# Optimization experiments

Measured on AMD Instinct MI355X. Metric: run time of the kernel, lower is better.

## Reference

```python
import jax, jax.numpy as jnp
import numpy as np

N, E, IN, H, OUT = 50000, 600000, 256, 128, 40
EPS, GAMMA = 0.1, 0.1  # PyG AntiSymmetricConv defaults


def _build_norm(edge_index, n):
    # GCNConv normalization with added self loops: D^-1/2 (A+I) D^-1/2
    loops = jnp.arange(n, dtype=edge_index.dtype)
    src = jnp.concatenate([edge_index[0], loops])
    dst = jnp.concatenate([edge_index[1], loops])
    deg = jax.ops.segment_sum(jnp.ones(src.shape[0], dtype=jnp.float32), dst, num_segments=n)
    dinv = jnp.where(deg > 0, jax.lax.rsqrt(jnp.maximum(deg, 1e-12)), 0.0)
    return src, dst, dinv[src] * dinv[dst]


def _gcn(x, w, src, dst, norm, n):
    # GCNConv(bias=False): scatter normalized messages to target nodes
    m = (x @ w)[src] * norm[:, None]          # [E+N, d]
    return jax.ops.segment_sum(m, dst, num_segments=n)


def _antisym_conv(x, W, gcn_w, bias, src, dst, norm, num_iters):
    d = W.shape[0]
    aW = W - W.T - GAMMA * jnp.eye(d, dtype=W.dtype)  # antisymmetric weight
    n = x.shape[0]

    def step(h, _):
        upd = jnp.tanh(h @ aW.T + _gcn(h, gcn_w, src, dst, norm, n) + bias)
        return h + EPS * upd, None

    x, _ = jax.lax.scan(step, x, None, length=num_iters)
    return x


def setup_inputs() -> dict:
    key = jax.random.key(0)
    ks = jax.random.split(key, 16)
    s = lambda fan: 1.0 / np.sqrt(fan)
    return {
        "x": jax.random.normal(ks[0], (N, IN), dtype=jnp.float32),
        "edge_index": jax.random.randint(ks[1], (2, E), 0, N, dtype=jnp.int64),
        "w_hid": jax.random.normal(ks[2], (H, IN), dtype=jnp.float32) * s(IN),
        "b_hid": jax.random.normal(ks[3], (H,), dtype=jnp.float32) * s(IN),
        "W_a1": jax.random.normal(ks[4], (H, H), dtype=jnp.float32) * s(H),
        "gcn_w1": jax.random.normal(ks[5], (H, H), dtype=jnp.float32) * s(H),
        "b_a1": jax.random.normal(ks[6], (H,), dtype=jnp.float32) * s(H),
        "w_hid2": jax.random.normal(ks[7], (H // 2, H), dtype=jnp.float32) * s(H),
        "b_hid2": jax.random.normal(ks[8], (H // 2,), dtype=jnp.float32) * s(H),
        "W_a2": jax.random.normal(ks[9], (H // 2, H // 2), dtype=jnp.float32) * s(H // 2),
        "gcn_w2": jax.random.normal(ks[10], (H // 2, H // 2), dtype=jnp.float32) * s(H // 2),
        "b_a2": jax.random.normal(ks[11], (H // 2,), dtype=jnp.float32) * s(H // 2),
        "w_fc": jax.random.normal(ks[12], (OUT, H // 2), dtype=jnp.float32) * s(H // 2),
        "b_fc": jax.random.normal(ks[13], (OUT,), dtype=jnp.float32) * s(H // 2),
    }


def reference(x, edge_index, w_hid, b_hid, W_a1, gcn_w1, b_a1,
              w_hid2, b_hid2, W_a2, gcn_w2, b_a2, w_fc, b_fc):
    n = x.shape[0]
    src, dst, norm = _build_norm(edge_index, n)
    h = jax.nn.leaky_relu(x @ w_hid.T + b_hid)          # dropout is no-op in eval
    h = _antisym_conv(h, W_a1, gcn_w1, b_a1, src, dst, norm, num_iters=3)
    h = jax.nn.leaky_relu(h)
    h = jax.nn.leaky_relu(h @ w_hid2.T + b_hid2)
    h = _antisym_conv(h, W_a2, gcn_w2, b_a2, src, dst, norm, num_iters=1)
    out = h @ w_fc.T + b_fc
    return jax.nn.log_softmax(out, axis=1)
```

## Files before the change

kernel.cpp:

```cpp
#include <hip/hip_runtime.h>
#include <hip/hip_bf16.h>
#include <math.h>

typedef unsigned short u16;
typedef unsigned int   u32;
using short8  = __attribute__((ext_vector_type(8))) short;
using f32x4   = __attribute__((ext_vector_type(4))) float;

static constexpr int NNODE = 50000;
static constexpr int NEDGE = 600000;
static constexpr float EPSC   = 0.1f;
static constexpr float GAMMAC = 0.1f;

static constexpr int NTILE = (NNODE + 63) / 64;
static constexpr int GH    = 128;
static constexpr int NRNG  = 12500;
static constexpr int NWORD = NRNG / 2;
static constexpr int NPASS = 4;

static constexpr long long O_DINV   = 0;
static constexpr long long O_DEGI   = 50000;
static constexpr long long O_ROWPTR = 100000;
static constexpr long long O_GCUR   = 150004;
static constexpr long long O_ECSR   = 200260;
static constexpr long long O_WHB    = 1400260;
static constexpr long long O_G1TB   = O_WHB  + 16384;
static constexpr long long O_AW1B   = O_G1TB + 8192;
static constexpr long long O_W2B    = O_AW1B + 8192;
static constexpr long long O_AW2B   = O_W2B  + 4096;
static constexpr long long O_G2TB   = O_AW2B + 2048;
static constexpr long long O_WFCB   = O_G2TB + 2048;
static constexpr long long O_AGGB   = 3450004;
static constexpr long long O_HB0    = O_AGGB + 3200000;
static constexpr long long O_HB1    = O_HB0  + 3200000;
static constexpr long long O_S0     = O_HB1  + 3200000;
static constexpr long long O_S1     = O_S0   + 1600000;
static constexpr long long O_PART   = O_S1   + 1600000;
static constexpr long long O_BASE   = O_PART + 3200000;

__device__ __forceinline__ float bf2f(u16 u) {
    return __uint_as_float(((unsigned)u) << 16);
}
__device__ __forceinline__ u16 f2bf(float f) {
    unsigned u = __float_as_uint(f);
    return (u16)((u + 0x7FFFu + ((u >> 16) & 1u)) >> 16);
}
__device__ __forceinline__ float ftanh(float x) {
    float x2 = fminf(fmaxf(2.f * x, -30.f), 30.f);
    float e = __expf(x2);
    return (e - 1.f) * __builtin_amdgcn_rcpf(e + 1.f);
}
__device__ __forceinline__ u16 pk_fp8(float a, float b) {
    int pk = __builtin_amdgcn_cvt_pk_fp8_f32(a, b, 0, false);
    return (u16)(pk & 0xffff);
}
__device__ __forceinline__ void acc_fp8x4(float* a, u32 v, float w) {
    a[0] += __builtin_amdgcn_cvt_f32_fp8(v, 0) * w;
    a[1] += __builtin_amdgcn_cvt_f32_fp8(v, 1) * w;
    a[2] += __builtin_amdgcn_cvt_f32_fp8(v, 2) * w;
    a[3] += __builtin_amdgcn_cvt_f32_fp8(v, 3) * w;
}

__global__ __launch_bounds__(256) void prep_kernel(
    const float* __restrict__ w_hid, const float* __restrict__ W_a1,
    const float* __restrict__ gcn1,  const float* __restrict__ w2,
    const float* __restrict__ W_a2,  const float* __restrict__ gcn2,
    const float* __restrict__ wfc,   float* __restrict__ ws)
{
    int j = blockIdx.x * 256 + threadIdx.x;
    if (j < 32768) { ((u16*)(ws+O_WHB))[j] = f2bf(w_hid[j]); return; } j -= 32768;
    if (j < 16384) { int r=j>>7, c=j&127; ((u16*)(ws+O_G1TB))[j] = f2bf(gcn1[c*128+r]); return; } j -= 16384;
    if (j < 16384) { int r=j>>7, c=j&127;
                     ((u16*)(ws+O_AW1B))[j] = f2bf(W_a1[r*128+c] - W_a1[c*128+r] - (r==c?GAMMAC:0.f));
                     return; } j -= 16384;
    if (j < 8192)  { ((u16*)(ws+O_W2B))[j] = f2bf(w2[j]); return; } j -= 8192;
    if (j < 4096)  { int r=j>>6, c=j&63;
                     ((u16*)(ws+O_AW2B))[j] = f2bf(W_a2[r*64+c] - W_a2[c*64+r] - (r==c?GAMMAC:0.f));
                     return; } j -= 4096;
    if (j < 4096)  { int r=j>>6, c=j&63; ((u16*)(ws+O_G2TB))[j] = f2bf(gcn2[c*64+r]); return; } j -= 4096;
    if (j < 2560)  { ((u16*)(ws+O_WFCB))[j] = f2bf(wfc[j]); return; } j -= 2560;
    if (j == 0)    { ((int*)(ws+O_GCUR))[0] = 0; }
}

__global__ __launch_bounds__(256) void alloc_kernel(
    const u16* __restrict__ part, float* __restrict__ dinv,
    int* __restrict__ degi, int* __restrict__ rowptr,
    u16* __restrict__ base16, int* __restrict__ gcur)
{
    int i = blockIdx.x * 256 + threadIdx.x;
    int lane = threadIdx.x & 63;
    bool ok = i < NNODE;
    int deg = 0;
    if (ok) {
        int run = 0;
        #pragma unroll 4
        for (int g = 0; g < GH; ++g) {
            base16[(long long)g * NNODE + i] = (u16)run;
            run += part[(long long)g * NNODE + i];
        }
        deg = run;
        degi[i] = deg;
        dinv[i] = rsqrtf(1.0f + (float)deg);
    }
    int run = deg;
    #pragma unroll
    for (int off = 1; off < 64; off <<= 1) {
        int v = __shfl_up(run, off);
        if (lane >= off) run += v;
    }
    int tot = __shfl(run, 63);
    int basep = 0;
    if (lane == 63) basep = atomicAdd(gcur, tot);
    basep = __shfl(basep, 63);
    if (ok) rowptr[i] = basep + run - deg;
}

__global__ __launch_bounds__(256) void fill_kernel(
    const int* __restrict__ ei, const float* __restrict__ dinv,
    const int* __restrict__ rowptr, const u16* __restrict__ base16,
    int2* __restrict__ ecsr)
{
    __shared__ u32 cur[NWORD];
    const int g    = blockIdx.x >> 2;
    const int pass = blockIdx.x & 3;
    const long long e0 = (long long)g * NEDGE / GH;
    const long long e1 = (long long)(g + 1) * NEDGE / GH;
    const u16* bb = base16 + (long long)g * NNODE;
    const int nbase = pass * NRNG;
    for (int wi = threadIdx.x; wi < NWORD; wi += 256) cur[wi] = 0;
    __syncthreads();
    for (long long e = e0 + threadIdx.x; e < e1; e += 256) {
        int d = ei[NEDGE + e];
        int r = d - nbase;
        if ((unsigned)r < (unsigned)NRNG) {
            int s = ei[e];
            u32 old = atomicAdd(&cur[r >> 1], 1u << ((r & 1) * 16));
            int rank = (int)((old >> ((r & 1) * 16)) & 0xffffu);
            int slot = rowptr[d] + (int)bb[d] + rank;
            int2 v;
            v.x = s;
            v.y = __float_as_int(dinv[s]);
            ecsr[slot] = v;
        }
    }
}

template<int KS, int NT, int AF32, int LOADACT, int EPI>
__global__ __launch_bounds__(256, 4) void mgemm(
    const void* __restrict__ Araw,
    const u16* __restrict__ Bt,
    const float* __restrict__ bias,
    float* __restrict__ outF,
    u16* __restrict__ outB,
    u16* __restrict__ outB8,
    int M, int Nn, int ldc,
    const int* __restrict__ ei,
    u16* __restrict__ partial)
{
    constexpr int K    = KS * 32;
    constexpr int KCHU = (K > 128) ? 128 : K;
    constexpr int KC   = KCHU / 32;
    constexpr int NCH  = K / KCHU;
    constexpr int P    = KCHU + 8;
    constexpr int ROWS = NT * 16;
    constexpr int CW   = NT * 16 + 1;
    constexpr int BSZ  = ROWS * P * 2;
    constexpr int ASZ  = 64 * CW * 4;
    constexpr int SMEM = BSZ > ASZ ? BSZ : ASZ;
    __shared__ __align__(16) char smem[SMEM];

    if (ei && blockIdx.x >= NTILE) {
        int g = blockIdx.x - NTILE;
        u32* hist = (u32*)smem;
        const long long e0 = (long long)g * NEDGE / GH;
        const long long e1 = (long long)(g + 1) * NEDGE / GH;
        u16* part = partial + (long long)g * NNODE;
        for (int pass = 0; pass < NPASS; ++pass) {
            const int nbase = pass * NRNG;
            for (int wi = threadIdx.x; wi < NWORD; wi += 256) hist[wi] = 0;
            __syncthreads();
            for (long long e = e0 + threadIdx.x; e < e1; e += 256) {
                int d = ei[NEDGE + e];
                int r = d - nbase;
                if ((unsigned)r < (unsigned)NRNG)
                    atomicAdd(&hist[r >> 1], 1u << ((r & 1) * 16));
            }
            __syncthreads();
            for (int wi = threadIdx.x; wi < NWORD; wi += 256)
                *(u32*)&part[nbase + wi * 2] = hist[wi];
            __syncthreads();
        }
        return;
    }

    u16*   bl   = (u16*)smem;
    float* accL = (float*)smem;

    const int wave = threadIdx.x >> 6;
    const int lane = threadIdx.x & 63;
    const int m = lane & 15, q = lane >> 4;
    const int rowbase = blockIdx.x * 64 + wave * 16;
    const int row = rowbase + m;
    const bool rok = row < M;
    const short8 z8 = {0,0,0,0,0,0,0,0};

    short8 af[KS];
    if (AF32) {
        const float* apf = (const float*)Araw + (long long)row * K;
        #pragma unroll
        for (int k = 0; k < KS; ++k) {
            short8 t = z8;
            if (rok) {
                const float4* p = (const float4*)(apf + (k * 4 + q) * 8);
                float4 a = p[0], b = p[1];
                t[0]=(short)f2bf(a.x); t[1]=(short)f2bf(a.y); t[2]=(short)f2bf(a.z); t[3]=(short)f2bf(a.w);
                t[4]=(short)f2bf(b.x); t[5]=(short)f2bf(b.y); t[6]=(short)f2bf(b.z); t[7]=(short)f2bf(b.w);
            }
            af[k] = t;
        }
    } else {
        const short8* ap = (const short8*)((const u16*)Araw + (long long)row * K);
        #pragma unroll
        for (int k = 0; k < KS; ++k) af[k] = rok ? ap[k * 4 + q] : z8;
    }
    if (LOADACT) {
        #pragma unroll
        for (int k = 0; k < KS; ++k)
            #pragma unroll
            for (int e = 0; e < 8; ++e) {
                float f = bf2f((u16)af[k][e]);
                f = f > 0.f ? f : 0.01f * f;
                af[k][e] = (short)f2bf(f);
            }
    }

    f32x4 acc[NT];
    #pragma unroll
    for (int j = 0; j < NT; ++j) acc[j] = (f32x4){0.f,0.f,0.f,0.f};

    for (int ch = 0; ch < NCH; ++ch) {
        if (ch) __syncthreads();
        constexpr int CHUNKS = ROWS * (KCHU / 8);
        for (int t = threadIdx.x; t < CHUNKS; t += 256) {
            int r = t / (KCHU / 8), c = t - r * (KCHU / 8);
            short8 v = z8;
            if (r < Nn) v = *(const short8*)&Bt[(long long)r * K + ch * KCHU + c * 8];
            *(short8*)&bl[r * P + c * 8] = v;
        }
        __syncthreads();
        #pragma unroll
        for (int j = 0; j < NT; ++j) {
            #pragma unroll
            for (int k = 0; k < KC; ++k) {
                short8 bf_ = *(const short8*)&bl[(j * 16 + m) * P + k * 32 + q * 8];
                acc[j] = __builtin_amdgcn_mfma_f32_16x16x32_bf16(af[ch * KC + k], bf_, acc[j], 0, 0, 0);
            }
        }
    }

    __syncthreads();
    #pragma unroll
    for (int j = 0; j < NT; ++j)
        #pragma unroll
        for (int r = 0; r < 4; ++r)
            accL[(wave * 16 + q * 4 + r) * CW + j * 16 + m] = acc[j][r];
    __syncthreads();

    const int c0 = lane * 2;
    if (c0 < NT * 16) {
        float2 bv = {0.f, 0.f};
        if (bias) {
            if (c0 < Nn)     bv.x = bias[c0];
            if (c0 + 1 < Nn) bv.y = bias[c0 + 1];
        }
        #pragma unroll
        for (int rl = 0; rl < 16; ++rl) {
            int rowD = rowbase + rl;
            if (rowD >= M) continue;
            float2 v = *(const float2*)&accL[(wave * 16 + rl) * CW + c0];
            long long o = (long long)rowD * ldc + c0;
            v.x += bv.x; v.y += bv.y;
            if (EPI == 1) {
                v.x = v.x > 0.f ? v.x : 0.01f * v.x;
                v.y = v.y > 0.f ? v.y : 0.01f * v.y;
            }
            if (c0 + 1 < Nn) {
                if (outB) { ushort2 ob; ob.x = f2bf(v.x); ob.y = f2bf(v.y);
                            *(ushort2*)&outB[o] = ob; }
                if (outB8) outB8[o >> 1] = pk_fp8(v.x, v.y);
                if (outF) { *(float2*)&outF[o] = v; }
            } else if (c0 < Nn) {
                if (outB) outB[o] = f2bf(v.x);
                if (outF) outF[o] = v.x;
            }
        }
    }
}

template<int HD>
__global__ __launch_bounds__(256) void gather_kernel(
    const int* __restrict__ rowptr, const int* __restrict__ degi,
    const int2* __restrict__ ecsr, const float* __restrict__ dinv,
    const u32* __restrict__ g8, u16* __restrict__ aggB)
{
    int node = (blockIdx.x * 256 + threadIdx.x) >> 6;
    int lane = threadIdx.x & 63;
    if (node >= NNODE) return;
    const int qr = lane >> 4, l4 = lane & 15;
    const int r0 = rowptr[node];
    const int r1 = r0 + degi[node];
    const float dn = dinv[node];
    constexpr int EL = (HD == 128) ? 8 : 4;

    float a[EL];
    #pragma unroll
    for (int i = 0; i < EL; ++i) a[i] = 0.f;
    if (qr == 0) {
        if (HD == 128) {
            uint2 gv = ((const uint2*)g8)[(long long)node * 16 + l4];
            acc_fp8x4(a, gv.x, dn);
            acc_fp8x4(a + 4, gv.y, dn);
        } else {
            u32 gv = g8[(long long)node * 16 + l4];
            acc_fp8x4(a, gv, dn);
        }
    }

    for (int base = r0; base < r1; base += 64) {
        int idx = base + lane;
        int cs = 0; float cw = 0.f;
        if (idx < r1) { int2 ev = ecsr[idx]; cs = ev.x; cw = __int_as_float(ev.y); }
        int cnt = min(64, r1 - base);
        for (int j = 0; j < cnt; j += 16) {
            #pragma unroll
            for (int u = 0; u < 4; ++u) {
                int jj = j + u * 4 + qr;
                int   s = __shfl(cs, jj);
                float w = __shfl(cw, jj);
                if (HD == 128) {
                    uint2 gv = ((const uint2*)g8)[(long long)s * 16 + l4];
                    acc_fp8x4(a, gv.x, w);
                    acc_fp8x4(a + 4, gv.y, w);
                } else {
                    u32 gv = g8[(long long)s * 16 + l4];
                    acc_fp8x4(a, gv, w);
                }
            }
        }
    }

    #pragma unroll
    for (int i = 0; i < EL; ++i) {
        a[i] += __shfl_xor(a[i], 16);
        a[i] += __shfl_xor(a[i], 32);
    }
    if (HD == 128) {
        float v0 = (qr == 0) ? a[0] : (qr == 1) ? a[2] : (qr == 2) ? a[4] : a[6];
        float v1 = (qr == 0) ? a[1] : (qr == 1) ? a[3] : (qr == 2) ? a[5] : a[7];
        v0 *= dn; v1 *= dn;
        long long o = (long long)node * 128 + l4 * 8 + qr * 2;
        ushort2 ob; ob.x = f2bf(v0); ob.y = f2bf(v1);
        *(ushort2*)&aggB[o] = ob;
    } else {
        float v = (qr == 0) ? a[0] : (qr == 1) ? a[1] : (qr == 2) ? a[2] : a[3];
        aggB[(long long)node * 64 + l4 * 4 + qr] = f2bf(v * dn);
    }
}

template<int TAIL>
__global__ __launch_bounds__(512, 3) void fconv(
    const u16* __restrict__ hA, const u32* __restrict__ g8,
    const int* __restrict__ rowptr, const int* __restrict__ degi,
    const int2* __restrict__ ecsr, const float* __restrict__ dinv,
    const u16* __restrict__ BtW, const u16* __restrict__ BtG,
    const float* __restrict__ bias,
    u16* __restrict__ outB, u16* __restrict__ outB8,
    const u16* __restrict__ w2W, const float* __restrict__ b2)
{
    constexpr int K = 128, P = 136;
    __shared__ __align__(16) char smem[52224];
    u16* bl   = (u16*)smem;
    u16* aggT = (u16*)(smem + 34816);
    const int wave = threadIdx.x >> 6, lane = threadIdx.x & 63;
    const int m = lane & 15, q = lane >> 4;
    const int blockrow = blockIdx.x * 64;
    const short8 z8 = {0,0,0,0,0,0,0,0};

    {
        const int qr = q, l4 = m;
        for (int nn = 0; nn < 8; ++nn) {
            int lr = wave * 8 + nn;
            int node = blockrow + lr;
            if (node >= NNODE) break;
            const int r0 = rowptr[node];
            const int r1 = r0 + degi[node];
            const float dn = dinv[node];
            float a[8] = {0.f,0.f,0.f,0.f,0.f,0.f,0.f,0.f};
            if (qr == 0) {
                uint2 gv = ((const uint2*)g8)[(long long)node * 16 + l4];
                acc_fp8x4(a, gv.x, dn);
                acc_fp8x4(a + 4, gv.y, dn);
            }
            for (int base = r0; base < r1; base += 64) {
                int idx = base + lane;
                int cs = 0; float cw = 0.f;
                if (idx < r1) { int2 ev = ecsr[idx]; cs = ev.x; cw = __int_as_float(ev.y); }
                int cnt = min(64, r1 - base);
                for (int j = 0; j < cnt; j += 16) {
                    #pragma unroll
                    for (int u = 0; u < 4; ++u) {
                        int jj = j + u * 4 + qr;
                        int   s = __shfl(cs, jj);
                        float w = __shfl(cw, jj);
                        uint2 gv = ((const uint2*)g8)[(long long)s * 16 + l4];
                        acc_fp8x4(a, gv.x, w);
                        acc_fp8x4(a + 4, gv.y, w);
                    }
                }
            }
            #pragma unroll
            for (int i = 0; i < 8; ++i) {
                a[i] += __shfl_xor(a[i], 16);
                a[i] += __shfl_xor(a[i], 32);
            }
            float v0 = (qr == 0) ? a[0] : (qr == 1) ? a[2] : (qr == 2) ? a[4] : a[6];
            float v1 = (qr == 0) ? a[1] : (qr == 1) ? a[3] : (qr == 2) ? a[5] : a[7];
            v0 *= dn; v1 *= dn;
            ushort2 ob; ob.x = f2bf(v0); ob.y = f2bf(v1);
            *(ushort2*)&aggT[lr * P + l4 * 8 + qr * 2] = ob;
        }
    }
    __syncthreads();

    const int nh = wave >> 2;
    const int rowbase = blockrow + (wave & 3) * 16;
    const int row = rowbase + m;
    const bool rok = row < NNODE;

    short8 af1[4], af2[4];
    {
        const short8* ap1 = (const short8*)(hA + (long long)row * K);
        #pragma unroll
        for (int k = 0; k < 4; ++k) {
            af1[k] = rok ? ap1[k * 4 + q] : z8;
            af2[k] = rok ? *(const short8*)&aggT[((wave & 3) * 16 + m) * P + k * 32 + q * 8] : z8;
        }
    }

    f32x4 acc[4];
    #pragma unroll
    for (int j = 0; j < 4; ++j) acc[j] = (f32x4){0.f,0.f,0.f,0.f};

    #pragma unroll
    for (int pass = 0; pass < 2; ++pass) {
        const u16* Bsrc = pass ? BtG : BtW;
        if (pass) __syncthreads();
        for (int t = threadIdx.x; t < 2048; t += 512) {
            int r = t >> 4, c = t & 15;
            *(short8*)&bl[r * P + c * 8] = *(const short8*)&Bsrc[(long long)r * K + c * 8];
        }
        __syncthreads();
        #pragma unroll
        for (int j = 0; j < 4; ++j)
            #pragma unroll
            for (int kk = 0; kk < 4; ++kk) {
                short8 b_ = *(const short8*)&bl[(nh*64 + j*16 + m) * P + kk*32 + q*8];
                acc[j] = __builtin_amdgcn_mfma_f32_16x16x32_bf16(
                    pass ? af2[kk] : af1[kk], b_, acc[j], 0, 0, 0);
            }
    }

    __syncthreads();
    float* accW = (float*)smem + wave * 16 * 65;
    #pragma unroll
    for (int j = 0; j < 4; ++j)
        #pragma unroll
        for (int r = 0; r < 4; ++r)
            accW[(q*4 + r) * 65 + j*16 + m] = acc[j][r];

    const int hw = lane >> 5;
    const int c0 = (lane & 31) * 2;
    float2 bv = {bias[nh*64 + c0], bias[nh*64 + c0 + 1]};

    if (TAIL == 0) {
        #pragma unroll
        for (int rl8 = 0; rl8 < 8; ++rl8) {
            int rl = hw * 8 + rl8;
            int rowD = rowbase + rl;
            if (rowD >= NNODE) continue;
            float2 v = *(const float2*)&accW[rl * 65 + c0];
            long long o = (long long)rowD * 128 + nh*64 + c0;
            ushort2 hh = *(const ushort2*)&hA[o];
            float n0 = bf2f(hh.x) + EPSC * ftanh(v.x + bv.x);
            float n1 = bf2f(hh.y) + EPSC * ftanh(v.y + bv.y);
            ushort2 ob; ob.x = f2bf(n0); ob.y = f2bf(n1);
            *(ushort2*)&outB[o] = ob;
            outB8[o >> 1] = pk_fp8(n0, n1);
        }
        return;
    }

    #pragma unroll
    for (int rl8 = 0; rl8 < 8; ++rl8) {
        int rl = hw * 8 + rl8;
        int rowD = rowbase + rl;
        float n0 = 0.f, n1 = 0.f;
        if (rowD < NNODE) {
            float2 v = *(const float2*)&accW[rl * 65 + c0];
            long long o = (long long)rowD * 128 + nh*64 + c0;
            ushort2 hh = *(const ushort2*)&hA[o];
            n0 = bf2f(hh.x) + EPSC * ftanh(v.x + bv.x);
            n1 = bf2f(hh.y) + EPSC * ftanh(v.y + bv.y);
            n0 = n0 > 0.f ? n0 : 0.01f * n0;
            n1 = n1 > 0.f ? n1 : 0.01f * n1;
        }
        ushort2 ob; ob.x = f2bf(n0); ob.y = f2bf(n1);
        *(ushort2*)&aggT[((wave & 3) * 16 + rl) * P + nh*64 + c0] = ob;
    }
    __syncthreads();

    short8 af3[4];
    #pragma unroll
    for (int k = 0; k < 4; ++k)
        af3[k] = *(const short8*)&aggT[((wave & 3) * 16 + m) * P + k * 32 + q * 8];

    for (int t = threadIdx.x; t < 1024; t += 512) {
        int r = t >> 4, c = t & 15;
        *(short8*)&bl[r * P + c * 8] = *(const short8*)&w2W[(long long)r * K + c * 8];
    }
    __syncthreads();

    f32x4 acc2[2];
    #pragma unroll
    for (int j = 0; j < 2; ++j) acc2[j] = (f32x4){0.f,0.f,0.f,0.f};
    #pragma unroll
    for (int j = 0; j < 2; ++j)
        #pragma unroll
        for (int k = 0; k < 4; ++k) {
            short8 b_ = *(const short8*)&bl[(nh*32 + j*16 + m) * P + k*32 + q*8];
            acc2[j] = __builtin_amdgcn_mfma_f32_16x16x32_bf16(af3[k], b_, acc2[j], 0, 0, 0);
        }

    __syncthreads();
    float* accW2 = (float*)smem + wave * 16 * 33;
    #pragma unroll
    for (int j = 0; j < 2; ++j)
        #pragma unroll
        for (int r = 0; r < 4; ++r)
            accW2[(q*4 + r) * 33 + j*16 + m] = acc2[j][r];

    const int r4 = lane >> 4;
    const int c2 = (lane & 15) * 2;
    float2 bv2 = {b2[nh*32 + c2], b2[nh*32 + c2 + 1]};
    #pragma unroll
    for (int rr = 0; rr < 4; ++rr) {
        int rl = r4 * 4 + rr;
        int rowD = rowbase + rl;
        if (rowD >= NNODE) continue;
        float2 v = *(const float2*)&accW2[rl * 33 + c2];
        v.x += bv2.x; v.y += bv2.y;
        v.x = v.x > 0.f ? v.x : 0.01f * v.x;
        v.y = v.y > 0.f ? v.y : 0.01f * v.y;
        long long o = (long long)rowD * 64 + nh*32 + c2;
        ushort2 ob; ob.x = f2bf(v.x); ob.y = f2bf(v.y);
        *(ushort2*)&outB[o] = ob;
        outB8[o >> 1] = pk_fp8(v.x, v.y);
    }
}

__global__ __launch_bounds__(256, 4) void conv2fc(
    const u16* __restrict__ hA,
    const u16* __restrict__ gA,
    const u16* __restrict__ BtW, const u16* __restrict__ BtG,
    const float* __restrict__ bias,
    const u16* __restrict__ wfcB, const float* __restrict__ bfc,
    float* __restrict__ outF, int M)
{
    constexpr int K  = 64, NT = 4, KS = 2;
    constexpr int P  = K + 8;
    constexpr int CW = 65;
    constexpr int R1 = 64 * CW * 4;
    __shared__ __align__(16) char smem[R1 + 64 * P * 2];
    u16*   bl   = (u16*)smem;
    float* accL = (float*)smem;
    u16*   aggT = (u16*)(smem + R1);

    const int wave = threadIdx.x >> 6;
    const int lane = threadIdx.x & 63;
    const int m = lane & 15, q = lane >> 4;
    const int rowbase = blockIdx.x * 64 + wave * 16;
    const int row = rowbase + m;
    const bool rok = row < M;
    const short8 z8 = {0,0,0,0,0,0,0,0};

    short8 af1[KS], af2[KS];
    {
        const short8* ap1 = (const short8*)(hA + (long long)row * K);
        const short8* ap2 = (const short8*)(gA + (long long)row * K);
        #pragma unroll
        for (int k = 0; k < KS; ++k) {
            af1[k] = rok ? ap1[k * 4 + q] : z8;
            af2[k] = rok ? ap2[k * 4 + q] : z8;
        }
    }

    f32x4 acc[NT];
    #pragma unroll
    for (int j = 0; j < NT; ++j) acc[j] = (f32x4){0.f,0.f,0.f,0.f};

    #pragma unroll
    for (int pass = 0; pass < 2; ++pass) {
        const u16* Bcur = pass ? BtG : BtW;
        if (pass) __syncthreads();
        constexpr int CHUNKS = 64 * (K / 8);
        for (int t = threadIdx.x; t < CHUNKS; t += 256) {
            int r = t >> 3, c = t & 7;
            *(short8*)&bl[r * P + c * 8] = *(const short8*)&Bcur[(long long)r * K + c * 8];
        }
        __syncthreads();
        #pragma unroll
        for (int j = 0; j < NT; ++j)
            #pragma unroll
            for (int k = 0; k < KS; ++k) {
                short8 bf_ = *(const short8*)&bl[(j * 16 + m) * P + k * 32 + q * 8];
                acc[j] = __builtin_amdgcn_mfma_f32_16x16x32_bf16(
                    pass ? af2[k] : af1[k], bf_, acc[j], 0, 0, 0);
            }
    }

    __syncthreads();
    #pragma unroll
    for (int j = 0; j < NT; ++j)
        #pragma unroll
        for (int r = 0; r < 4; ++r)
            accL[(wave * 16 + q * 4 + r) * CW + j * 16 + m] = acc[j][r];
    __syncthreads();

    {
        const int c0 = lane * 2;
        float2 bv = {bias[c0 & 63], bias[(c0 + 1) & 63]};
        if (c0 < 64) {
            #pragma unroll
            for (int rl = 0; rl < 16; ++rl) {
                int rowD = rowbase + rl;
                float n0 = 0.f, n1 = 0.f;
                if (rowD < M) {
                    float2 v = *(const float2*)&accL[(wave * 16 + rl) * CW + c0];
                    long long o = (long long)rowD * 64 + c0;
                    ushort2 hh = *(const ushort2*)&hA[o];
                    n0 = bf2f(hh.x) + EPSC * ftanh(v.x + bv.x);
                    n1 = bf2f(hh.y) + EPSC * ftanh(v.y + bv.y);
                }
                ushort2 ob; ob.x = f2bf(n0); ob.y = f2bf(n1);
                *(ushort2*)&aggT[(wave * 16 + rl) * P + c0] = ob;
            }
        }
    }
    __syncthreads();

    short8 af4[KS];
    #pragma unroll
    for (int k = 0; k < KS; ++k)
        af4[k] = *(const short8*)&aggT[(wave * 16 + m) * P + k * 32 + q * 8];

    {
        constexpr int CHF = 48 * 8;
        for (int t = threadIdx.x; t < CHF; t += 256) {
            int r = t >> 3, c = t & 7;
            short8 v = z8;
            if (r < 40) v = *(const short8*)&wfcB[(long long)r * K + c * 8];
            *(short8*)&bl[r * P + c * 8] = v;
        }
    }
    __syncthreads();

    f32x4 acc3[3];
    #pragma unroll
    for (int j = 0; j < 3; ++j) acc3[j] = (f32x4){0.f,0.f,0.f,0.f};
    #pragma unroll
    for (int j = 0; j < 3; ++j)
        #pragma unroll
        for (int k = 0; k < KS; ++k) {
            short8 bf_ = *(const short8*)&bl[(j * 16 + m) * P + k * 32 + q * 8];
            acc3[j] = __builtin_amdgcn_mfma_f32_16x16x32_bf16(af4[k], bf_, acc3[j], 0, 0, 0);
        }

    __syncthreads();
    constexpr int CW3 = 49;
    #pragma unroll
    for (int j = 0; j < 3; ++j)
        #pragma unroll
        for (int r = 0; r < 4; ++r)
            accL[(wave * 16 + q * 4 + r) * CW3 + j * 16 + m] = acc3[j][r];
    __syncthreads();

    float mrow = 0.f, lrow = 0.f;
    if (lane < 16) {
        const float* rp = &accL[(wave * 16 + lane) * CW3];
        float mx = -1e30f;
        for (int c = 0; c < 40; ++c) mx = fmaxf(mx, rp[c] + bfc[c]);
        float s = 0.f;
        for (int c = 0; c < 40; ++c) s += expf(rp[c] + bfc[c] - mx);
        mrow = mx; lrow = logf(s);
    }
    for (int rl = 0; rl < 16; ++rl) {
        float mm = __shfl(mrow, rl);
        float ll = __shfl(lrow, rl);
        int rowD = rowbase + rl;
        if (rowD < M && lane < 40) {
            float v = accL[(wave * 16 + rl) * CW3 + lane] + bfc[lane];
            outF[(long long)rowD * 40 + lane] = v - mm - ll;
        }
    }
}

extern "C" void kernel_launch(void* const* d_in, const int* in_sizes, int n_in,
                              void* d_out, int out_size, void* d_ws, size_t ws_size,
                              hipStream_t stream) {
    const float* x     = (const float*)d_in[0];
    const int*   ei    = (const int*)d_in[1];
    const float* w_hid = (const float*)d_in[2];
    const float* b_hid = (const float*)d_in[3];
    const float* W_a1  = (const float*)d_in[4];
    const float* gcn1  = (const float*)d_in[5];
    const float* b_a1  = (const float*)d_in[6];
    const float* w2    = (const float*)d_in[7];
    const float* b2    = (const float*)d_in[8];
    const float* W_a2  = (const float*)d_in[9];
    const float* gcn2  = (const float*)d_in[10];
    const float* b_a2  = (const float*)d_in[11];
    const float* wfc   = (const float*)d_in[12];
    const float* bfc   = (const float*)d_in[13];
    float* ws = (float*)d_ws;
    float* out = (float*)d_out;

    float* dinv   = ws + O_DINV;
    int*   degi   = (int*)(ws + O_DEGI);
    int*   rowptr = (int*)(ws + O_ROWPTR);
    int*   gcur   = (int*)(ws + O_GCUR);
    int2*  ecsr   = (int2*)(ws + O_ECSR);
    u16* whB  = (u16*)(ws + O_WHB);
    u16* g1tB = (u16*)(ws + O_G1TB);
    u16* aw1B = (u16*)(ws + O_AW1B);
    u16* w2B  = (u16*)(ws + O_W2B);
    u16* aw2B = (u16*)(ws + O_AW2B);
    u16* g2tB = (u16*)(ws + O_G2TB);
    u16* wfcB = (u16*)(ws + O_WFCB);
    u16* aggB = (u16*)(ws + O_AGGB);
    u16* hB0  = (u16*)(ws + O_HB0);
    u16* hB1  = (u16*)(ws + O_HB1);
    u16* s0   = (u16*)(ws + O_S0);
    u16* s1   = (u16*)(ws + O_S1);
    u16* part = (u16*)(ws + O_PART);
    u16* base16 = (u16*)(ws + O_BASE);

    prep_kernel<<<(84481 + 255) / 256, 256, 0, stream>>>(
        w_hid, W_a1, gcn1, w2, W_a2, gcn2, wfc, ws);

    const int gatherBlocks = (NNODE * 64 + 255) / 256;

    mgemm<8, 8, 1, 0, 1><<<NTILE + GH, 256, 0, stream>>>(
        x, whB, b_hid, nullptr, hB0, s0, NNODE, 128, 128, ei, part);

    alloc_kernel<<<(NNODE + 255) / 256, 256, 0, stream>>>(
        part, dinv, degi, rowptr, base16, gcur);
    fill_kernel<<<GH * NPASS, 256, 0, stream>>>(ei, dinv, rowptr, base16, ecsr);

    fconv<0><<<NTILE, 512, 0, stream>>>(hB0, (const u32*)s0, rowptr, degi, ecsr, dinv,
                                        aw1B, g1tB, b_a1, hB1, s1, nullptr, nullptr);
    fconv<0><<<NTILE, 512, 0, stream>>>(hB1, (const u32*)s1, rowptr, degi, ecsr, dinv,
                                        aw1B, g1tB, b_a1, hB0, s0, nullptr, nullptr);
    fconv<1><<<NTILE, 512, 0, stream>>>(hB0, (const u32*)s0, rowptr, degi, ecsr, dinv,
                                        aw1B, g1tB, b_a1, hB1, s1, w2B, b2);

    gather_kernel<64><<<gatherBlocks, 256, 0, stream>>>(
        rowptr, degi, ecsr, dinv, (const u32*)s1, aggB);
    conv2fc<<<NTILE, 256, 0, stream>>>(
        hB1, aggB, aw2B, g2tB, b_a2, wfcB, bfc, out, NNODE);
}
```

Baseline: 355.9 us.

## Split weight staging into K-halves to shrink LDS and raise occupancy to 4

The fused conv kernel now stages each 128x128 weight matrix into shared memory in two 64-column K-halves with a narrower pitch. That cuts the LDS footprint from about 51KB to 35KB, and launch bounds are raised to 4 blocks per CU to use the freed space for more resident waves. The TAIL path holds its results in registers across an extra barrier, because the smaller layout can overlap the accumulator scratch with aggT. The cost is more barriers per block and a tighter register budget, which may cause spills.

```diff
diff --git a/kernel.cpp b/kernel.cpp
--- a/kernel.cpp
+++ b/kernel.cpp
@@ -368,7 +368,7 @@
 }
 
 template<int TAIL>
-__global__ __launch_bounds__(512, 3) void fconv(
+__global__ __launch_bounds__(512, 4) void fconv(
     const u16* __restrict__ hA, const u32* __restrict__ g8,
     const int* __restrict__ rowptr, const int* __restrict__ degi,
     const int2* __restrict__ ecsr, const float* __restrict__ dinv,
@@ -377,10 +377,10 @@
     u16* __restrict__ outB, u16* __restrict__ outB8,
     const u16* __restrict__ w2W, const float* __restrict__ b2)
 {
-    constexpr int K = 128, P = 136;
-    __shared__ __align__(16) char smem[52224];
+    constexpr int K = 128, PB = 72, PA = 136;
+    __shared__ __align__(16) char smem[35840];
     u16* bl   = (u16*)smem;
-    u16* aggT = (u16*)(smem + 34816);
+    u16* aggT = (u16*)(smem + 18432);
     const int wave = threadIdx.x >> 6, lane = threadIdx.x & 63;
     const int m = lane & 15, q = lane >> 4;
     const int blockrow = blockIdx.x * 64;
@@ -427,7 +427,7 @@
             float v1 = (qr == 0) ? a[1] : (qr == 1) ? a[3] : (qr == 2) ? a[5] : a[7];
             v0 *= dn; v1 *= dn;
             ushort2 ob; ob.x = f2bf(v0); ob.y = f2bf(v1);
-            *(ushort2*)&aggT[lr * P + l4 * 8 + qr * 2] = ob;
+            *(ushort2*)&aggT[lr * PA + l4 * 8 + qr * 2] = ob;
         }
     }
     __syncthreads();
@@ -443,7 +443,7 @@
         #pragma unroll
         for (int k = 0; k < 4; ++k) {
             af1[k] = rok ? ap1[k * 4 + q] : z8;
-            af2[k] = rok ? *(const short8*)&aggT[((wave & 3) * 16 + m) * P + k * 32 + q * 8] : z8;
+            af2[k] = rok ? *(const short8*)&aggT[((wave & 3) * 16 + m) * PA + k * 32 + q * 8] : z8;
         }
     }
 
@@ -452,21 +452,23 @@
     for (int j = 0; j < 4; ++j) acc[j] = (f32x4){0.f,0.f,0.f,0.f};
 
     #pragma unroll
-    for (int pass = 0; pass < 2; ++pass) {
+    for (int ph = 0; ph < 4; ++ph) {
+        const int pass = ph >> 1, ch = ph & 1;
         const u16* Bsrc = pass ? BtG : BtW;
-        if (pass) __syncthreads();
-        for (int t = threadIdx.x; t < 2048; t += 512) {
-            int r = t >> 4, c = t & 15;
-            *(short8*)&bl[r * P + c * 8] = *(const short8*)&Bsrc[(long long)r * K + c * 8];
+        if (ph) __syncthreads();
+        for (int t = threadIdx.x; t < 1024; t += 512) {
+            int r = t >> 3, c = t & 7;
+            *(short8*)&bl[r * PB + c * 8] =
+                *(const short8*)&Bsrc[(long long)r * K + ch*64 + c*8];
         }
         __syncthreads();
         #pragma unroll
         for (int j = 0; j < 4; ++j)
             #pragma unroll
-            for (int kk = 0; kk < 4; ++kk) {
-                short8 b_ = *(const short8*)&bl[(nh*64 + j*16 + m) * P + kk*32 + q*8];
+            for (int kk = 0; kk < 2; ++kk) {
+                short8 b_ = *(const short8*)&bl[(nh*64 + j*16 + m) * PB + kk*32 + q*8];
                 acc[j] = __builtin_amdgcn_mfma_f32_16x16x32_bf16(
-                    pass ? af2[kk] : af1[kk], b_, acc[j], 0, 0, 0);
+                    pass ? af2[2*ch + kk] : af1[2*ch + kk], b_, acc[j], 0, 0, 0);
             }
     }
 
@@ -500,6 +502,7 @@
         return;
     }
 
+    u32 hv[8];
     #pragma unroll
     for (int rl8 = 0; rl8 < 8; ++rl8) {
         int rl = hw * 8 + rl8;
@@ -514,32 +517,43 @@
             n0 = n0 > 0.f ? n0 : 0.01f * n0;
             n1 = n1 > 0.f ? n1 : 0.01f * n1;
         }
-        ushort2 ob; ob.x = f2bf(n0); ob.y = f2bf(n1);
-        *(ushort2*)&aggT[((wave & 3) * 16 + rl) * P + nh*64 + c0] = ob;
+        hv[rl8] = (u32)f2bf(n0) | ((u32)f2bf(n1) << 16);
+    }
+    __syncthreads();
+
+    #pragma unroll
+    for (int rl8 = 0; rl8 < 8; ++rl8) {
+        int rl = hw * 8 + rl8;
+        *(u32*)&aggT[((wave & 3) * 16 + rl) * PA + nh*64 + c0] = hv[rl8];
     }
     __syncthreads();
 
     short8 af3[4];
     #pragma unroll
     for (int k = 0; k < 4; ++k)
-        af3[k] = *(const short8*)&aggT[((wave & 3) * 16 + m) * P + k * 32 + q * 8];
-
-    for (int t = threadIdx.x; t < 1024; t += 512) {
-        int r = t >> 4, c = t & 15;
-        *(short8*)&bl[r * P + c * 8] = *(const short8*)&w2W[(long long)r * K + c * 8];
-    }
-    __syncthreads();
+        af3[k] = *(const short8*)&aggT[((wave & 3) * 16 + m) * PA + k * 32 + q * 8];
 
     f32x4 acc2[2];
     #pragma unroll
     for (int j = 0; j < 2; ++j) acc2[j] = (f32x4){0.f,0.f,0.f,0.f};
     #pragma unroll
-    for (int j = 0; j < 2; ++j)
-        #pragma unroll
-        for (int k = 0; k < 4; ++k) {
-            short8 b_ = *(const short8*)&bl[(nh*32 + j*16 + m) * P + k*32 + q*8];
-            acc2[j] = __builtin_amdgcn_mfma_f32_16x16x32_bf16(af3[k], b_, acc2[j], 0, 0, 0);
-        }
+    for (int ch = 0; ch < 2; ++ch) {
+        if (ch) __syncthreads();
+        for (int t = threadIdx.x; t < 512; t += 512) {
+            int r = t >> 3, c = t & 7;
+            *(short8*)&bl[r * PB + c * 8] =
+                *(const short8*)&w2W[(long long)r * K + ch*64 + c*8];
+        }
+        __syncthreads();
+        #pragma unroll
+        for (int j = 0; j < 2; ++j)
+            #pragma unroll
+            for (int kk = 0; kk < 2; ++kk) {
+                short8 b_ = *(const short8*)&bl[(nh*32 + j*16 + m) * PB + kk*32 + q*8];
+                acc2[j] = __builtin_amdgcn_mfma_f32_16x16x32_bf16(
+                    af3[2*ch + kk], b_, acc2[j], 0, 0, 0);
+            }
+    }
 
     __syncthreads();
     float* accW2 = (float*)smem + wave * 16 * 33;
```

Result: slower. 363.4 us (+2.1%).
